# Kernel tuning notes

Hardware: AMD Instinct MI355X
Metric: run time of the kernel (lower is better)

## Reference

```python
import jax, jax.numpy as jnp
import numpy as np

# DeepSeek MLA prefill pipeline (absorbed form), matching the GEMM/bmm/sparse-attention
# Dims: m=512 tokens, hidden=7168, d_kv_c=512, d_q_c=1536, d_r=64, d_q=d_kv=128,
# h=16 local heads, attention dim d = d_kv_c + d_r = 576, s_kv=4096, topk=512.

M, HID = 512, 7168
D_KV_C, D_Q_C, D_R, D_Q, D_KV = 512, 1536, 64, 128, 128
H = 16
S_KV, TOPK = 4096, 512
D_ATT = D_KV_C + D_R  # 576


def setup_inputs() -> dict:
    key = jax.random.key(0)
    ks = jax.random.split(key, 8)
    s = lambda n: 1.0 / np.sqrt(n).astype(np.float32)
    return {
        "x": jax.random.normal(ks[0], (M, HID), jnp.float32),
        "W_cqkv": jax.random.normal(ks[1], (HID, D_KV_C + D_Q_C + D_R), jnp.float32) * s(HID),
        "W_uq": jax.random.normal(ks[2], (D_Q_C, H * (D_Q + D_R)), jnp.float32) * s(D_Q_C),
        "W_qk": jax.random.normal(ks[3], (H, D_Q, D_KV_C), jnp.float32) * s(D_Q),
        "kv_cache": jax.random.normal(ks[4], (S_KV, D_ATT), jnp.float32),
        "W_o1": jax.random.normal(ks[5], (H, D_KV_C, D_KV), jnp.float32) * s(D_KV_C),
        "W_oproj": jax.random.normal(ks[6], (H * D_KV, HID), jnp.float32) * s(H * D_KV),
        "indices": jax.random.randint(ks[7], (M, TOPK), 0, S_KV, jnp.int32),
    }


def reference(x, W_cqkv, W_uq, W_qk, kv_cache, W_o1, W_oproj, indices):
    # 1) QKV compression GEMM: [m, hid] @ [hid, d_kv_c + d_q_c + d_r]
    c = x @ W_cqkv
    kv_c_new = c[:, :D_KV_C]                      # compressed KV (would extend cache)
    q_c = c[:, D_KV_C:D_KV_C + D_Q_C]             # [m, d_q_c]
    # (kv_c_new / k_r_new feed the cache in a real pipeline; attention below reads

    # 2) Q uncompression GEMM: [m, d_q_c] @ [d_q_c, h*(d_q+d_r)]
    q = (q_c @ W_uq).reshape(M, H, D_Q + D_R)
    q_nope, q_pe = q[..., :D_Q], q[..., D_Q:]     # [m,h,128], [m,h,64]

    # 3) Q absorb bmm: per-head [m, d_q] @ [d_q, d_kv_c]
    q_abs = jnp.einsum('mhq,hqc->mhc', q_nope, W_qk)
    q_full = jnp.concatenate([q_abs, q_pe], axis=-1)  # [m, h, 576]

    # 4) Top-k sparse MLA attention (flash_mla_sparse_fwd math):
    #    indices shared across heads (h_kv = 1); gather kv rows per query token.
    kv_g = kv_cache[indices]                      # [m, topk, 576]
    sm_scale = 1.0 / jnp.sqrt(jnp.float32(D_ATT))
    scores = jnp.einsum('mhd,mtd->mht', q_full, kv_g) * sm_scale
    attn = jax.nn.softmax(scores, axis=-1)        # [m, h, topk]
    o = jnp.einsum('mht,mtc->mhc', attn, kv_g[..., :D_KV_C])  # value = first d_kv_c dims

    # 5) O bmm: per-head [m, d_kv_c] @ [d_kv_c, d_kv]
    o2 = jnp.einsum('mhc,hcv->mhv', o, W_o1)      # [m, h, 128]

    # 6) O projection GEMM: [m, h*d_kv] @ [h*d_kv, hid]
    out = o2.reshape(M, H * D_KV) @ W_oproj       # [m, hid]
    return out
```

## Files before the change

kernel.cpp:

```cpp
#include <hip/hip_runtime.h>
#include <hip/hip_bf16.h>

#define M_DIM 512
#define HID 7168
#define D_KV_C 512
#define D_Q_C 1536
#define D_R 64
#define D_Q 128
#define D_KV 128
#define H_DIM 16
#define S_KV 4096
#define TOPK 512
#define D_ATT 576

typedef _Float16 half_t;
typedef __attribute__((ext_vector_type(8))) _Float16 f16x8_t;
typedef __attribute__((ext_vector_type(4))) float f32x4_t;
typedef __attribute__((ext_vector_type(2))) unsigned int u32x2_t;

#define MFMA_F16(a, b, c) __builtin_amdgcn_mfma_f32_16x16x32_f16((a), (b), (c), 0, 0, 0)

__device__ __forceinline__ unsigned lds_addr32(const void* p) {
    return (unsigned)(unsigned long long)(const __attribute__((address_space(3))) char*)p;
}

typedef const __attribute__((address_space(1))) unsigned int* gptr_t;
typedef __attribute__((address_space(3))) unsigned int* lptr_t;
__device__ __forceinline__ void gload_lds16(const void* g, void* l) {
    __builtin_amdgcn_global_load_lds((gptr_t)g, (lptr_t)l, 16, 0, 0);
}

__global__ __launch_bounds__(256) void cvt_f16(const float* __restrict__ src,
                                               half_t* __restrict__ dst, int n8)
{
    int i = blockIdx.x * 256 + threadIdx.x;
    if (i >= n8) return;
    const float4* s = (const float4*)src + (size_t)i * 2;
    float4 a = s[0], b = s[1];
    f16x8_t o;
    o[0] = (half_t)a.x; o[1] = (half_t)a.y; o[2] = (half_t)a.z; o[3] = (half_t)a.w;
    o[4] = (half_t)b.x; o[5] = (half_t)b.y; o[6] = (half_t)b.z; o[7] = (half_t)b.w;
    *(f16x8_t*)(dst + (size_t)i * 8) = o;
}

template<int NS>
__global__ __launch_bounds__(256) void cvt_sum(const float* __restrict__ src, long long slice,
                                               half_t* __restrict__ dst, int n8)
{
    int i = blockIdx.x * 256 + threadIdx.x;
    if (i >= n8) return;
    float a[8] = {};
    #pragma unroll
    for (int s = 0; s < NS; s++) {
        const float4* p = (const float4*)(src + (size_t)s * slice) + (size_t)i * 2;
        float4 u = p[0], v = p[1];
        a[0] += u.x; a[1] += u.y; a[2] += u.z; a[3] += u.w;
        a[4] += v.x; a[5] += v.y; a[6] += v.z; a[7] += v.w;
    }
    f16x8_t o;
    #pragma unroll
    for (int j = 0; j < 8; j++) o[j] = (half_t)a[j];
    *(f16x8_t*)(dst + (size_t)i * 8) = o;
}

__global__ __launch_bounds__(256) void cvt_sum_q(const float* __restrict__ src, long long slice,
                                                 half_t* __restrict__ q16, half_t* __restrict__ qf)
{
    int i = blockIdx.x * 256 + threadIdx.x;
    if (i >= M_DIM * 3072 / 8) return;
    float a[8] = {};
    #pragma unroll
    for (int s = 0; s < 2; s++) {
        const float4* p = (const float4*)(src + (size_t)s * slice) + (size_t)i * 2;
        float4 u = p[0], v = p[1];
        a[0] += u.x; a[1] += u.y; a[2] += u.z; a[3] += u.w;
        a[4] += v.x; a[5] += v.y; a[6] += v.z; a[7] += v.w;
    }
    f16x8_t o;
    #pragma unroll
    for (int j = 0; j < 8; j++) o[j] = (half_t)a[j];
    *(f16x8_t*)(q16 + (size_t)i * 8) = o;
    int col = (i * 8) % 3072;
    int c = col % 192;
    if (c >= 128) {
        int row = (i * 8) / 3072, h = col / 192;
        int mh = row * 16 + h;
        *(f16x8_t*)(qf + (size_t)mh * D_ATT + D_KV_C + (c - 128)) = o;
    }
}

__global__ __launch_bounds__(256) void cvt_t(
    const float* __restrict__ src, int ld_src, long long sS,
    half_t* __restrict__ dst, int ld_dst, long long sD)
{
    src += (size_t)blockIdx.z * sS;
    dst += (size_t)blockIdx.z * sD;
    int k0 = blockIdx.y * 64, n0 = blockIdx.x * 64;
    __shared__ half_t t[64][80];
    int tid = threadIdx.x;
    int kr = tid >> 4, nc = (tid & 15) * 4;
    #pragma unroll
    for (int i = 0; i < 4; i++) {
        float4 v = *(const float4*)&src[(size_t)(k0 + kr + i * 16) * ld_src + n0 + nc];
        t[nc + 0][kr + i * 16] = (half_t)v.x;
        t[nc + 1][kr + i * 16] = (half_t)v.y;
        t[nc + 2][kr + i * 16] = (half_t)v.z;
        t[nc + 3][kr + i * 16] = (half_t)v.w;
    }
    __syncthreads();
    int nr = tid >> 2, kc = (tid & 3) * 16;
    f16x8_t w0 = *(const f16x8_t*)&t[nr][kc];
    f16x8_t w1 = *(const f16x8_t*)&t[nr][kc + 8];
    *(f16x8_t*)&dst[(size_t)(n0 + nr) * ld_dst + k0 + kc] = w0;
    *(f16x8_t*)&dst[(size_t)(n0 + nr) * ld_dst + k0 + kc + 8] = w1;
}

template<bool F16OUT>
__global__ __launch_bounds__(256) void gemm_f16t(
    const half_t* __restrict__ A, int lda, long long sA,
    const half_t* __restrict__ Bt, int ldb, long long sB,
    void* __restrict__ Cv, int ldc, long long sC, int K)
{
    A  += (size_t)blockIdx.z * sA;
    Bt += (size_t)blockIdx.z * sB;
    const int bm = blockIdx.y * 64, bn = blockIdx.x * 64;

    __shared__ __align__(16) char lds[2][16384];

    const int tid = threadIdx.x, w = tid >> 6, lane = tid & 63;
    const int l15 = lane & 15, q = lane >> 4;
    const int wr = w >> 1, wc = w & 1;

    const half_t* gA[2];
    const half_t* gB[2];
    #pragma unroll
    for (int p = 0; p < 2; p++) {
        int c = p * 64 + lane;
        int rl = c >> 3;
        int sg = (c & 7) ^ (rl & 7);
        gA[p] = A  + (size_t)(bm + w * 16 + rl) * lda + sg * 8;
        gB[p] = Bt + (size_t)(bn + w * 16 + rl) * ldb + sg * 8;
    }

    f32x4_t acc[2][2];
    #pragma unroll
    for (int i = 0; i < 2; i++)
        #pragma unroll
        for (int j = 0; j < 2; j++) acc[i][j] = (f32x4_t){0.f, 0.f, 0.f, 0.f};

    const int nsteps = K >> 6;

    {
        char* ab = lds[0];
        char* bb = ab + 8192;
        #pragma unroll
        for (int p = 0; p < 2; p++) {
            gload_lds16(gA[p], ab + w * 2048 + p * 1024);
            gload_lds16(gB[p], bb + w * 2048 + p * 1024);
        }
    }
    __syncthreads();

    int cur = 0;
    for (int s = 0; s < nsteps; s++) {
        if (s + 1 < nsteps) {
            int k0 = (s + 1) << 6;
            char* ab = lds[cur ^ 1];
            char* bb = ab + 8192;
            #pragma unroll
            for (int p = 0; p < 2; p++) {
                gload_lds16(gA[p] + k0, ab + w * 2048 + p * 1024);
                gload_lds16(gB[p] + k0, bb + w * 2048 + p * 1024);
            }
        }
        {
            const char* ab = lds[cur];
            const char* bb = ab + 8192;
            #pragma unroll
            for (int kk = 0; kk < 2; kk++) {
                f16x8_t av[2], bv[2];
                #pragma unroll
                for (int i = 0; i < 2; i++) {
                    int ra = wr * 32 + i * 16 + l15;
                    av[i] = *(const f16x8_t*)(ab + ra * 128 + (((kk * 4 + q) ^ (ra & 7)) * 16));
                    int rb = wc * 32 + i * 16 + l15;
                    bv[i] = *(const f16x8_t*)(bb + rb * 128 + (((kk * 4 + q) ^ (rb & 7)) * 16));
                }
                #pragma unroll
                for (int i = 0; i < 2; i++)
                    #pragma unroll
                    for (int j = 0; j < 2; j++)
                        acc[i][j] = MFMA_F16(av[i], bv[j], acc[i][j]);
            }
        }
        __syncthreads();
        cur ^= 1;
    }

    half_t* Ch = (half_t*)Cv + (F16OUT ? (size_t)blockIdx.z * sC : 0);
    float*  Cf = (float*)Cv  + (F16OUT ? 0 : (size_t)blockIdx.z * sC);
    #pragma unroll
    for (int i = 0; i < 2; i++)
        #pragma unroll
        for (int j = 0; j < 2; j++)
            #pragma unroll
            for (int r = 0; r < 4; r++) {
                size_t row = bm + wr * 32 + i * 16 + q * 4 + r;
                size_t col = bn + wc * 32 + j * 16 + l15;
                if (F16OUT) Ch[row * ldc + col] = (half_t)acc[i][j][r];
                else        Cf[row * ldc + col] = acc[i][j][r];
            }
}

__global__ __launch_bounds__(256) void attn_mfma(
    const half_t* __restrict__ qf,
    const half_t* __restrict__ kvb,
    const int* __restrict__ indices,
    half_t* __restrict__ o)
{
    const int m = blockIdx.x;
    const int tid = threadIdx.x;
    const int w = tid >> 6, lane = tid & 63;
    const int l15 = lane & 15, q = lane >> 4;

    __shared__ __align__(16) char u_mem[16 * 513 * 4];
    __shared__ __align__(16) unsigned short p_s[16 * 512];
    __shared__ int idx_s[TOPK];

    float* s_s = (float*)u_mem;
    unsigned short* v_s = (unsigned short*)u_mem;

    for (int i = tid; i < TOPK; i += 256) idx_s[i] = indices[(size_t)m * TOPK + i];
    __syncthreads();

    int rows[8];
    #pragma unroll
    for (int tt = 0; tt < 8; tt++) rows[tt] = idx_s[(w * 8 + tt) * 16 + l15];

    f32x4_t acc[8];
    #pragma unroll
    for (int tt = 0; tt < 8; tt++) acc[tt] = (f32x4_t){0.f, 0.f, 0.f, 0.f};

    const half_t* qh = qf + ((size_t)m * 16 + l15) * D_ATT + q * 8;

    #pragma unroll 2
    for (int kk = 0; kk < 18; kk++) {
        f16x8_t ah = *(const f16x8_t*)(qh + kk * 32);
        #pragma unroll
        for (int tt = 0; tt < 8; tt++) {
            f16x8_t b = *(const f16x8_t*)(kvb + (size_t)rows[tt] * D_ATT + kk * 32 + q * 8);
            acc[tt] = MFMA_F16(ah, b, acc[tt]);
        }
    }

    const float scale = 1.0f / 24.0f;
    #pragma unroll
    for (int tt = 0; tt < 8; tt++) {
        int t = (w * 8 + tt) * 16 + l15;
        #pragma unroll
        for (int r = 0; r < 4; r++)
            s_s[(q * 4 + r) * 513 + t] = acc[tt][r] * scale;
    }
    __syncthreads();

    {
        int h = tid >> 4, j = tid & 15;
        float mx = -1e30f;
        for (int t = j; t < TOPK; t += 16) mx = fmaxf(mx, s_s[h * 513 + t]);
        #pragma unroll
        for (int off = 8; off; off >>= 1) mx = fmaxf(mx, __shfl_xor(mx, off, 16));
        float sum = 0.f;
        for (int t = j; t < TOPK; t += 16) {
            float e = __expf(s_s[h * 513 + t] - mx);
            s_s[h * 513 + t] = e;
            sum += e;
        }
        #pragma unroll
        for (int off = 8; off; off >>= 1) sum += __shfl_xor(sum, off, 16);
        float inv = 1.0f / sum;
        for (int t = j; t < TOPK; t += 16) {
            union { half_t h; unsigned short u; } cv;
            cv.h = (half_t)(s_s[h * 513 + t] * inv);
            unsigned byte = ((unsigned)(t * 2)) ^ (((unsigned)(h & 7)) << 4);
            p_s[h * 512 + (byte >> 1)] = cv.u;
        }
    }
    __syncthreads();

    f32x4_t oacc[8];
    #pragma unroll
    for (int i = 0; i < 8; i++) oacc[i] = (f32x4_t){0.f, 0.f, 0.f, 0.f};

    const unsigned vbase = lds_addr32(v_s);
    const int jb = tid & 7, trow = tid >> 3;
    const unsigned swz_w = (((unsigned)(trow & 7)) << 4) ^ (((unsigned)((trow >> 3) & 3)) << 5);

    int rstage[16];
    #pragma unroll
    for (int ct = 0; ct < 16; ct++) rstage[ct] = idx_s[ct * 32 + trow];

    const int row1 = q * 8 + (l15 >> 2);
    const int row2 = row1 + 4;
    const unsigned sw1 = (((unsigned)(row1 & 7)) << 4) ^ (((unsigned)q & 3u) << 5);
    const unsigned sw2 = (((unsigned)(row2 & 7)) << 4) ^ (((unsigned)q & 3u) << 5);
    const unsigned cbyte = (unsigned)((l15 & 3) * 8);

    {
        const half_t* src = kvb + (size_t)rstage[0] * D_ATT + jb * 64;
        f16x8_t tmp[8];
        #pragma unroll
        for (int i = 0; i < 8; i++) tmp[i] = *(const f16x8_t*)(src + i * 8);
        #pragma unroll
        for (int i = 0; i < 8; i++) {
            unsigned byte = ((unsigned)(jb * 128 + i * 16)) ^ swz_w;
            *(f16x8_t*)((char*)v_s + trow * 1024 + byte) = tmp[i];
        }
    }
    __syncthreads();

    #pragma unroll 1
    for (int ct = 0; ct < 16; ct++) {
        int t0 = ct * 32;

        f16x8_t nxt[8];
        if (ct < 15) {
            const half_t* src = kvb + (size_t)rstage[ct + 1] * D_ATT + jb * 64;
            #pragma unroll
            for (int i = 0; i < 8; i++) nxt[i] = *(const f16x8_t*)(src + i * 8);
        }

        f16x8_t pa;
        {
            unsigned pbyte = ((unsigned)(t0 * 2 + q * 16)) ^ (((unsigned)(l15 & 7)) << 4);
            pa = *(const f16x8_t*)((const char*)p_s + l15 * 1024 + pbyte);
        }

        u32x2_t blo[8], bhi[8];
        #pragma unroll
        for (int i = 0; i < 8; i++) {
            unsigned c2 = ((unsigned)(((w * 8 + i) * 16) * 2)) + cbyte;
            unsigned a1 = vbase + (unsigned)row1 * 1024u + (c2 ^ sw1);
            unsigned a2 = vbase + (unsigned)row2 * 1024u + (c2 ^ sw2);
            asm volatile("ds_read_b64_tr_b16 %0, %1 offset:0" : "=v"(blo[i]) : "v"(a1) : "memory");
            asm volatile("ds_read_b64_tr_b16 %0, %1 offset:0" : "=v"(bhi[i]) : "v"(a2) : "memory");
        }
        asm volatile("s_waitcnt lgkmcnt(0)" ::: "memory");
        __builtin_amdgcn_sched_barrier(0);

        __builtin_amdgcn_s_setprio(1);
        #pragma unroll
        for (int i = 0; i < 8; i++) {
            union { f16x8_t s; struct { u32x2_t lo, hi; } u; } f;
            f.u.lo = blo[i]; f.u.hi = bhi[i];
            oacc[i] = MFMA_F16(pa, f.s, oacc[i]);
        }
        __builtin_amdgcn_s_setprio(0);

        __syncthreads();

        if (ct < 15) {
            #pragma unroll
            for (int i = 0; i < 8; i++) {
                unsigned byte = ((unsigned)(jb * 128 + i * 16)) ^ swz_w;
                *(f16x8_t*)((char*)v_s + trow * 1024 + byte) = nxt[i];
            }
        }
        __syncthreads();
    }

    half_t* ob = o + (size_t)m * (H_DIM * D_KV_C);
    #pragma unroll
    for (int i = 0; i < 8; i++) {
        int c = (w * 8 + i) * 16 + l15;
        #pragma unroll
        for (int r = 0; r < 4; r++)
            ob[(size_t)(q * 4 + r) * D_KV_C + c] = (half_t)oacc[i][r];
    }
}

extern "C" void kernel_launch(void* const* d_in, const int* in_sizes, int n_in,
                              void* d_out, int out_size, void* d_ws, size_t ws_size,
                              hipStream_t stream)
{
    const float* x        = (const float*)d_in[0];
    const float* W_cqkv   = (const float*)d_in[1];
    const float* W_uq     = (const float*)d_in[2];
    const float* W_qk     = (const float*)d_in[3];
    const float* kv_cache = (const float*)d_in[4];
    const float* W_o1     = (const float*)d_in[5];
    const float* W_oproj  = (const float*)d_in[6];
    const int*   indices  = (const int*)d_in[7];
    float* out = (float*)d_out;

    half_t* wsh = (half_t*)d_ws;
    half_t* Wcqkv_t = wsh;
    half_t* qc16    = wsh;
    half_t* q32h    = wsh + 786432;
    half_t* q16     = wsh + 7077888;
    half_t* x16     = wsh + 11010048;
    half_t* o2_16   = wsh + 11010048;
    half_t* Wuq_t   = wsh + 14680064;
    half_t* o16     = wsh + 14680064;
    half_t* Wqk_t   = wsh + 19398656;
    half_t* Wo1_t   = wsh + 20447232;
    half_t* Wop_t   = wsh + 21495808;
    half_t* kv16    = wsh + 36175872;
    half_t* qc32h   = wsh + 38535168;
    half_t* qf16    = wsh + 38535168;
    float* qc32 = (float*)qc32h;
    float* q32  = (float*)q32h;

    cvt_f16<<<(M_DIM * HID / 8 + 255) / 256, 256, 0, stream>>>(x, x16, M_DIM * HID / 8);
    cvt_f16<<<(S_KV * D_ATT / 8 + 255) / 256, 256, 0, stream>>>(kv_cache, kv16, S_KV * D_ATT / 8);
    cvt_t<<<dim3(D_Q_C / 64, HID / 64, 1), 256, 0, stream>>>(
        W_cqkv + D_KV_C, D_KV_C + D_Q_C + D_R, 0, Wcqkv_t, HID, 0);
    cvt_t<<<dim3(3072 / 64, D_Q_C / 64, 1), 256, 0, stream>>>(
        W_uq, 3072, 0, Wuq_t, D_Q_C, 0);
    cvt_t<<<dim3(D_KV_C / 64, D_Q / 64, H_DIM), 256, 0, stream>>>(
        W_qk, D_KV_C, D_Q * D_KV_C, Wqk_t, D_Q, D_Q * D_KV_C);
    cvt_t<<<dim3(D_KV / 64, D_KV_C / 64, H_DIM), 256, 0, stream>>>(
        W_o1, D_KV, D_KV_C * D_KV, Wo1_t, D_KV_C, D_KV_C * D_KV);
    cvt_t<<<dim3(HID / 64, 2048 / 64, 1), 256, 0, stream>>>(
        W_oproj, HID, 0, Wop_t, 2048, 0);

    gemm_f16t<false><<<dim3(D_Q_C / 64, M_DIM / 64, 4), 256, 0, stream>>>(
        x16, HID, 1792, Wcqkv_t, HID, 1792, qc32, D_Q_C, (long long)M_DIM * D_Q_C, 1792);
    cvt_sum<4><<<(M_DIM * D_Q_C / 8 + 255) / 256, 256, 0, stream>>>(
        qc32, (long long)M_DIM * D_Q_C, qc16, M_DIM * D_Q_C / 8);

    gemm_f16t<false><<<dim3(3072 / 64, M_DIM / 64, 2), 256, 0, stream>>>(
        qc16, D_Q_C, 768, Wuq_t, D_Q_C, 768, q32, 3072, (long long)M_DIM * 3072, 768);
    cvt_sum_q<<<(M_DIM * 3072 / 8 + 255) / 256, 256, 0, stream>>>(
        q32, (long long)M_DIM * 3072, q16, qf16);

    gemm_f16t<true><<<dim3(D_KV_C / 64, M_DIM / 64, H_DIM), 256, 0, stream>>>(
        q16, 3072, D_Q + D_R, Wqk_t, D_Q, (long long)D_Q * D_KV_C,
        qf16, H_DIM * D_ATT, D_ATT, D_Q);

    attn_mfma<<<M_DIM, 256, 0, stream>>>(qf16, kv16, indices, o16);

    gemm_f16t<true><<<dim3(D_KV / 64, M_DIM / 64, H_DIM), 256, 0, stream>>>(
        o16, H_DIM * D_KV_C, D_KV_C, Wo1_t, D_KV_C, (long long)D_KV_C * D_KV,
        o2_16, H_DIM * D_KV, D_KV, D_KV_C);

    gemm_f16t<false><<<dim3(HID / 64, M_DIM / 64, 1), 256, 0, stream>>>(
        o2_16, H_DIM * D_KV, 0, Wop_t, 2048, 0, out, HID, 0, H_DIM * D_KV);
}
```

Measured before the change: 221.4 us.

## Split sparse attention over top-k halves with 512-thread blocks and a merge kernel

The sparse attention kernel now splits each token's 512 top-k rows into two halves, one per block (grid M x 2) with 512 threads. Each half writes unnormalized partial outputs plus its row max and exp-sum, and a new merge kernel combines the two halves with log-sum-exp rescaling. The goal is more blocks and waves to hide gather latency. In exchange it adds a partial-output round trip through memory, an extra kernel launch, and drops the register double-buffering of V tiles.

```diff
diff --git a/kernel.cpp b/kernel.cpp
--- a/kernel.cpp
+++ b/kernel.cpp
@@ -12,6 +12,8 @@
 #define S_KV 4096
 #define TOPK 512
 #define D_ATT 576
+#define SPLIT 2
+#define SROWS 256
 
 typedef _Float16 half_t;
 typedef __attribute__((ext_vector_type(8))) _Float16 f16x8_t;
@@ -212,42 +214,41 @@
             }
 }
 
-__global__ __launch_bounds__(256) void attn_mfma(
+__global__ __launch_bounds__(512) void attn_split(
     const half_t* __restrict__ qf,
     const half_t* __restrict__ kvb,
     const int* __restrict__ indices,
-    half_t* __restrict__ o)
-{
-    const int m = blockIdx.x;
+    half_t* __restrict__ op,
+    float2* __restrict__ ml)
+{
+    const int m = blockIdx.x, sp = blockIdx.y;
     const int tid = threadIdx.x;
     const int w = tid >> 6, lane = tid & 63;
     const int l15 = lane & 15, q = lane >> 4;
 
-    __shared__ __align__(16) char u_mem[16 * 513 * 4];
-    __shared__ __align__(16) unsigned short p_s[16 * 512];
-    __shared__ int idx_s[TOPK];
+    __shared__ __align__(16) char u_mem[32768];
+    __shared__ __align__(16) unsigned short p_s[16 * SROWS];
 
     float* s_s = (float*)u_mem;
     unsigned short* v_s = (unsigned short*)u_mem;
 
-    for (int i = tid; i < TOPK; i += 256) idx_s[i] = indices[(size_t)m * TOPK + i];
-    __syncthreads();
-
-    int rows[8];
-    #pragma unroll
-    for (int tt = 0; tt < 8; tt++) rows[tt] = idx_s[(w * 8 + tt) * 16 + l15];
-
-    f32x4_t acc[8];
-    #pragma unroll
-    for (int tt = 0; tt < 8; tt++) acc[tt] = (f32x4_t){0.f, 0.f, 0.f, 0.f};
+    const int* idxp = indices + (size_t)m * TOPK + sp * SROWS;
+
+    int rows[2];
+    rows[0] = idxp[(w * 2 + 0) * 16 + l15];
+    rows[1] = idxp[(w * 2 + 1) * 16 + l15];
+
+    f32x4_t acc[2];
+    acc[0] = (f32x4_t){0.f, 0.f, 0.f, 0.f};
+    acc[1] = (f32x4_t){0.f, 0.f, 0.f, 0.f};
 
     const half_t* qh = qf + ((size_t)m * 16 + l15) * D_ATT + q * 8;
 
-    #pragma unroll 2
+    #pragma unroll 3
     for (int kk = 0; kk < 18; kk++) {
         f16x8_t ah = *(const f16x8_t*)(qh + kk * 32);
         #pragma unroll
-        for (int tt = 0; tt < 8; tt++) {
+        for (int tt = 0; tt < 2; tt++) {
             f16x8_t b = *(const f16x8_t*)(kvb + (size_t)rows[tt] * D_ATT + kk * 32 + q * 8);
             acc[tt] = MFMA_F16(ah, b, acc[tt]);
         }
@@ -255,49 +256,49 @@
 
     const float scale = 1.0f / 24.0f;
     #pragma unroll
-    for (int tt = 0; tt < 8; tt++) {
-        int t = (w * 8 + tt) * 16 + l15;
+    for (int tt = 0; tt < 2; tt++) {
+        int t = (w * 2 + tt) * 16 + l15;
         #pragma unroll
         for (int r = 0; r < 4; r++)
-            s_s[(q * 4 + r) * 513 + t] = acc[tt][r] * scale;
+            s_s[(q * 4 + r) * 260 + t] = acc[tt][r] * scale;
     }
     __syncthreads();
 
     {
-        int h = tid >> 4, j = tid & 15;
+        int h = tid >> 5, j = tid & 31;
         float mx = -1e30f;
-        for (int t = j; t < TOPK; t += 16) mx = fmaxf(mx, s_s[h * 513 + t]);
-        #pragma unroll
-        for (int off = 8; off; off >>= 1) mx = fmaxf(mx, __shfl_xor(mx, off, 16));
+        #pragma unroll
+        for (int t = j; t < SROWS; t += 32) mx = fmaxf(mx, s_s[h * 260 + t]);
+        #pragma unroll
+        for (int off = 16; off; off >>= 1) mx = fmaxf(mx, __shfl_xor(mx, off, 32));
         float sum = 0.f;
-        for (int t = j; t < TOPK; t += 16) {
-            float e = __expf(s_s[h * 513 + t] - mx);
-            s_s[h * 513 + t] = e;
+        #pragma unroll
+        for (int t = j; t < SROWS; t += 32) {
+            float e = __expf(s_s[h * 260 + t] - mx);
             sum += e;
-        }
-        #pragma unroll
-        for (int off = 8; off; off >>= 1) sum += __shfl_xor(sum, off, 16);
-        float inv = 1.0f / sum;
-        for (int t = j; t < TOPK; t += 16) {
-            union { half_t h; unsigned short u; } cv;
-            cv.h = (half_t)(s_s[h * 513 + t] * inv);
+            union { half_t hh; unsigned short u; } cv;
+            cv.hh = (half_t)e;
             unsigned byte = ((unsigned)(t * 2)) ^ (((unsigned)(h & 7)) << 4);
-            p_s[h * 512 + (byte >> 1)] = cv.u;
-        }
+            p_s[h * SROWS + (byte >> 1)] = cv.u;
+        }
+        #pragma unroll
+        for (int off = 16; off; off >>= 1) sum += __shfl_xor(sum, off, 32);
+        if (j == 0)
+            ml[(size_t)sp * (M_DIM * H_DIM) + m * 16 + h] = make_float2(mx, sum);
     }
     __syncthreads();
 
-    f32x4_t oacc[8];
-    #pragma unroll
-    for (int i = 0; i < 8; i++) oacc[i] = (f32x4_t){0.f, 0.f, 0.f, 0.f};
+    f32x4_t oacc[4];
+    #pragma unroll
+    for (int i = 0; i < 4; i++) oacc[i] = (f32x4_t){0.f, 0.f, 0.f, 0.f};
 
     const unsigned vbase = lds_addr32(v_s);
-    const int jb = tid & 7, trow = tid >> 3;
+    const int trow = tid >> 4, jb4 = tid & 15;
     const unsigned swz_w = (((unsigned)(trow & 7)) << 4) ^ (((unsigned)((trow >> 3) & 3)) << 5);
 
-    int rstage[16];
-    #pragma unroll
-    for (int ct = 0; ct < 16; ct++) rstage[ct] = idx_s[ct * 32 + trow];
+    int rstage[8];
+    #pragma unroll
+    for (int ct = 0; ct < 8; ct++) rstage[ct] = idxp[ct * 32 + trow];
 
     const int row1 = q * 8 + (l15 >> 2);
     const int row2 = row1 + 4;
@@ -305,40 +306,31 @@
     const unsigned sw2 = (((unsigned)(row2 & 7)) << 4) ^ (((unsigned)q & 3u) << 5);
     const unsigned cbyte = (unsigned)((l15 & 3) * 8);
 
-    {
-        const half_t* src = kvb + (size_t)rstage[0] * D_ATT + jb * 64;
-        f16x8_t tmp[8];
-        #pragma unroll
-        for (int i = 0; i < 8; i++) tmp[i] = *(const f16x8_t*)(src + i * 8);
-        #pragma unroll
-        for (int i = 0; i < 8; i++) {
-            unsigned byte = ((unsigned)(jb * 128 + i * 16)) ^ swz_w;
-            *(f16x8_t*)((char*)v_s + trow * 1024 + byte) = tmp[i];
-        }
-    }
-    __syncthreads();
-
     #pragma unroll 1
-    for (int ct = 0; ct < 16; ct++) {
-        int t0 = ct * 32;
-
-        f16x8_t nxt[8];
-        if (ct < 15) {
-            const half_t* src = kvb + (size_t)rstage[ct + 1] * D_ATT + jb * 64;
+    for (int ct = 0; ct < 8; ct++) {
+        {
+            const half_t* src = kvb + (size_t)rstage[ct] * D_ATT + jb4 * 32;
+            f16x8_t tmp[4];
             #pragma unroll
-            for (int i = 0; i < 8; i++) nxt[i] = *(const f16x8_t*)(src + i * 8);
-        }
+            for (int i = 0; i < 4; i++) tmp[i] = *(const f16x8_t*)(src + i * 8);
+            #pragma unroll
+            for (int i = 0; i < 4; i++) {
+                unsigned byte = ((unsigned)(jb4 * 64 + i * 16)) ^ swz_w;
+                *(f16x8_t*)((char*)v_s + trow * 1024 + byte) = tmp[i];
+            }
+        }
+        __syncthreads();
 
         f16x8_t pa;
         {
-            unsigned pbyte = ((unsigned)(t0 * 2 + q * 16)) ^ (((unsigned)(l15 & 7)) << 4);
-            pa = *(const f16x8_t*)((const char*)p_s + l15 * 1024 + pbyte);
-        }
-
-        u32x2_t blo[8], bhi[8];
-        #pragma unroll
-        for (int i = 0; i < 8; i++) {
-            unsigned c2 = ((unsigned)(((w * 8 + i) * 16) * 2)) + cbyte;
+            unsigned pbyte = ((unsigned)(ct * 64 + q * 16)) ^ (((unsigned)(l15 & 7)) << 4);
+            pa = *(const f16x8_t*)((const char*)p_s + l15 * (SROWS * 2) + pbyte);
+        }
+
+        u32x2_t blo[4], bhi[4];
+        #pragma unroll
+        for (int i = 0; i < 4; i++) {
+            unsigned c2 = ((unsigned)((w * 4 + i) * 32)) + cbyte;
             unsigned a1 = vbase + (unsigned)row1 * 1024u + (c2 ^ sw1);
             unsigned a2 = vbase + (unsigned)row2 * 1024u + (c2 ^ sw2);
             asm volatile("ds_read_b64_tr_b16 %0, %1 offset:0" : "=v"(blo[i]) : "v"(a1) : "memory");
@@ -349,7 +341,7 @@
 
         __builtin_amdgcn_s_setprio(1);
         #pragma unroll
-        for (int i = 0; i < 8; i++) {
+        for (int i = 0; i < 4; i++) {
             union { f16x8_t s; struct { u32x2_t lo, hi; } u; } f;
             f.u.lo = blo[i]; f.u.hi = bhi[i];
             oacc[i] = MFMA_F16(pa, f.s, oacc[i]);
@@ -357,25 +349,40 @@
         __builtin_amdgcn_s_setprio(0);
 
         __syncthreads();
-
-        if (ct < 15) {
-            #pragma unroll
-            for (int i = 0; i < 8; i++) {
-                unsigned byte = ((unsigned)(jb * 128 + i * 16)) ^ swz_w;
-                *(f16x8_t*)((char*)v_s + trow * 1024 + byte) = nxt[i];
-            }
-        }
-        __syncthreads();
-    }
-
-    half_t* ob = o + (size_t)m * (H_DIM * D_KV_C);
-    #pragma unroll
-    for (int i = 0; i < 8; i++) {
-        int c = (w * 8 + i) * 16 + l15;
+    }
+
+    half_t* ob = op + ((size_t)sp * M_DIM + m) * (H_DIM * D_KV_C);
+    #pragma unroll
+    for (int i = 0; i < 4; i++) {
+        int c = (w * 4 + i) * 16 + l15;
         #pragma unroll
         for (int r = 0; r < 4; r++)
             ob[(size_t)(q * 4 + r) * D_KV_C + c] = (half_t)oacc[i][r];
     }
+}
+
+__global__ __launch_bounds__(256) void attn_merge(
+    const half_t* __restrict__ op,
+    const float2* __restrict__ ml,
+    half_t* __restrict__ o)
+{
+    int idx = blockIdx.x * 256 + threadIdx.x;
+    if (idx >= M_DIM * H_DIM * D_KV_C / 8) return;
+    int mh = idx >> 6;
+    int c8 = (idx & 63) * 8;
+    float2 a = ml[mh];
+    float2 b = ml[M_DIM * H_DIM + mh];
+    float Mx = fmaxf(a.x, b.x);
+    float w0 = __expf(a.x - Mx), w1 = __expf(b.x - Mx);
+    float inv = 1.0f / (w0 * a.y + w1 * b.y);
+    w0 *= inv; w1 *= inv;
+    f16x8_t v0 = *(const f16x8_t*)(op + (size_t)mh * D_KV_C + c8);
+    f16x8_t v1 = *(const f16x8_t*)(op + ((size_t)(M_DIM * H_DIM) + mh) * D_KV_C + c8);
+    f16x8_t o8;
+    #pragma unroll
+    for (int j = 0; j < 8; j++)
+        o8[j] = (half_t)(w0 * (float)v0[j] + w1 * (float)v1[j]);
+    *(f16x8_t*)(o + (size_t)mh * D_KV_C + c8) = o8;
 }
 
 extern "C" void kernel_launch(void* const* d_in, const int* in_sizes, int n_in,
@@ -395,6 +402,7 @@
     half_t* wsh = (half_t*)d_ws;
     half_t* Wcqkv_t = wsh;
     half_t* qc16    = wsh;
+    half_t* o_part  = wsh;
     half_t* q32h    = wsh + 786432;
     half_t* q16     = wsh + 7077888;
     half_t* x16     = wsh + 11010048;
@@ -402,13 +410,16 @@
     half_t* Wuq_t   = wsh + 14680064;
     half_t* o16     = wsh + 14680064;
     half_t* Wqk_t   = wsh + 19398656;
+    half_t* ml_h    = wsh + 19398656;
     half_t* Wo1_t   = wsh + 20447232;
     half_t* Wop_t   = wsh + 21495808;
     half_t* kv16    = wsh + 36175872;
     half_t* qc32h   = wsh + 38535168;
     half_t* qf16    = wsh + 38535168;
-    float* qc32 = (float*)qc32h;
-    float* q32  = (float*)q32h;
+    float*  qc32 = (float*)qc32h;
+    float*  q32  = (float*)q32h;
+    float2* ml   = (float2*)ml_h;
+
 
     cvt_f16<<<(M_DIM * HID / 8 + 255) / 256, 256, 0, stream>>>(x, x16, M_DIM * HID / 8);
     cvt_f16<<<(S_KV * D_ATT / 8 + 255) / 256, 256, 0, stream>>>(kv_cache, kv16, S_KV * D_ATT / 8);
@@ -437,7 +448,8 @@
         q16, 3072, D_Q + D_R, Wqk_t, D_Q, (long long)D_Q * D_KV_C,
         qf16, H_DIM * D_ATT, D_ATT, D_Q);
 
-    attn_mfma<<<M_DIM, 256, 0, stream>>>(qf16, kv16, indices, o16);
+    attn_split<<<dim3(M_DIM, SPLIT), 512, 0, stream>>>(qf16, kv16, indices, o_part, ml);
+    attn_merge<<<(M_DIM * H_DIM * D_KV_C / 8 + 255) / 256, 256, 0, stream>>>(o_part, ml, o16);
 
     gemm_f16t<true><<<dim3(D_KV / 64, M_DIM / 64, H_DIM), 256, 0, stream>>>(
         o16, H_DIM * D_KV_C, D_KV_C, Wo1_t, D_KV_C, (long long)D_KV_C * D_KV,
```

Result: no change. 222.8 us (+0.6%).
